# Performance work log

Hardware: AMD Instinct MI355X
Metric: run time of the kernel (lower is better)

The kernel has to match this reference:

```python
import jax, jax.numpy as jnp
import numpy as np


def setup_inputs() -> dict:
    key = jax.random.key(0)
    B, T, H, W = 256, 16, 160, 160
    sms = 2
    N = T * (H // sms) * (W // sms)  # 102400 tokens per sample
    k1, _ = jax.random.split(key)
    soft_scores = jax.random.uniform(k1, (B, N), dtype=jnp.float32)
    image_grid_thw = jnp.tile(jnp.array([T, H, W], dtype=jnp.int64), (B, 1))
    return {
        "soft_scores": soft_scores,
        "image_grid_thw": image_grid_thw,
        "spatial_merge_size": sms,
    }


def reference(soft_scores, image_grid_thw, spatial_merge_size,
              lambda_compact=1.0, lambda_tv=1.0, eps=1e-6):
    if soft_scores.ndim == 3:
        soft_scores = soft_scores[..., 0]
    B = soft_scores.shape[0]
    # Uniform grid across the batch (static shapes) -> vectorize over B.
    thw = np.asarray(image_grid_thw)
    t = int(thw[0, 0])
    h = int(thw[0, 1]) // spatial_merge_size
    w = int(thw[0, 2]) // spatial_merge_size
    n = t * h * w

    # s: [B, t, h, w], clamped at 0 like torch clamp_min(0.0)
    s = jnp.maximum(soft_scores[:, :n].astype(jnp.float32).reshape(B, t, h, w), 0.0)
    tot = jnp.maximum(s.sum(axis=(1, 2, 3), keepdims=True), eps)
    p = s / tot  # per-sample normalized distribution

    yy = jnp.linspace(-1.0, 1.0, h, dtype=jnp.float32).reshape(1, 1, h, 1)
    xx = jnp.linspace(-1.0, 1.0, w, dtype=jnp.float32).reshape(1, 1, 1, w)
    mu_x = (p * xx).sum(axis=(1, 2, 3)).reshape(B, 1, 1, 1)
    mu_y = (p * yy).sum(axis=(1, 2, 3)).reshape(B, 1, 1, 1)
    compact = (p * ((xx - mu_x) ** 2 + (yy - mu_y) ** 2)).sum(axis=(1, 2, 3))  # [B]

    tv = jnp.zeros((B,), dtype=jnp.float32)
    if h > 1:
        tv = tv + jnp.abs(s[:, :, 1:, :] - s[:, :, :-1, :]).mean(axis=(1, 2, 3))
    if w > 1:
        tv = tv + jnp.abs(s[:, :, :, 1:] - s[:, :, :, :-1]).mean(axis=(1, 2, 3))
    if t > 1:
        tv = tv + 0.3 * jnp.abs(s[:, 1:, :, :] - s[:, :-1, :, :]).mean(axis=(1, 2, 3))

    return compact.mean() * lambda_compact + tv.mean() * lambda_tv
```

## Files before the change

kernel.cpp:

```cpp
#include <hip/hip_runtime.h>

#define T_DIM 16
#define H2 80
#define W2 80
#define SLICE (H2 * W2)
#define SAMPLE (T_DIM * SLICE)
#define BANDS 5
#define ROWS_PER_BAND (H2 / BANDS)
#define BLOCK (ROWS_PER_BAND * W2 / 4)

__device__ __forceinline__ float4 relu4(float4 v) {
    v.x = fmaxf(v.x, 0.f); v.y = fmaxf(v.y, 0.f);
    v.z = fmaxf(v.z, 0.f); v.w = fmaxf(v.w, 0.f);
    return v;
}

__global__ __launch_bounds__(BLOCK) void tsr_phase1(const float* __restrict__ scores,
                                                    float* __restrict__ ws) {
    __shared__ float lds[(ROWS_PER_BAND + 1) * W2];
    __shared__ float red[(BLOCK / 64) * 7];

    const int blk  = blockIdx.x;
    const int b    = blk / BANDS;
    const int band = blk % BANDS;
    const int tid  = threadIdx.x;

    const int y0  = band * ROWS_PER_BAND;
    const int r   = tid / (W2 / 4);
    const int cx  = tid % (W2 / 4);
    const int y   = y0 + r;
    const int xb  = cx * 4;
    const int pos = tid * 4;

    const float step = 2.0f / (float)(H2 - 1);
    const float yy  = -1.0f + (float)y * step;
    const float xx0 = -1.0f + (float)(xb + 0) * step;
    const float xx1 = -1.0f + (float)(xb + 1) * step;
    const float xx2 = -1.0f + (float)(xb + 2) * step;
    const float xx3 = -1.0f + (float)(xb + 3) * step;
    const float yy2 = yy * yy;
    const float cq0 = xx0 * xx0 + yy2;
    const float cq1 = xx1 * xx1 + yy2;
    const float cq2 = xx2 * xx2 + yy2;
    const float cq3 = xx3 * xx3 + yy2;

    const float4* base = (const float4*)(scores + (size_t)b * SAMPLE);
    const int f4idx = band * BLOCK + tid;
    const bool halo = (y0 + ROWS_PER_BAND < H2) && (tid < W2 / 4);
    const int haloIdx = (y0 + ROWS_PER_BAND) * (W2 / 4) + tid;

    const bool wavail = (xb + 4 < W2);
    const bool havail = (y + 1 < H2);

    float s0 = 0.f, sx = 0.f, sy = 0.f, sq = 0.f;
    float tvh = 0.f, tvw = 0.f, tvt = 0.f;
    float4 prev = make_float4(0.f, 0.f, 0.f, 0.f);

    float4 v = relu4(base[f4idx]);
    float4 hv = make_float4(0.f, 0.f, 0.f, 0.f);
    if (halo) hv = relu4(base[haloIdx]);

    for (int t = 0; t < T_DIM; ++t) {
        float4 vn = make_float4(0.f, 0.f, 0.f, 0.f);
        float4 hvn = make_float4(0.f, 0.f, 0.f, 0.f);
        if (t + 1 < T_DIM) {
            const float4* sln = base + (size_t)(t + 1) * (SLICE / 4);
            vn = sln[f4idx];
            if (halo) hvn = sln[haloIdx];
        }

        __syncthreads();
        *(float4*)&lds[pos] = v;
        if (halo) *(float4*)&lds[ROWS_PER_BAND * W2 + tid * 4] = hv;
        __syncthreads();

        const float rs = v.x + v.y + v.z + v.w;
        s0 += rs;
        sy = fmaf(yy, rs, sy);
        sx = fmaf(xx0, v.x, sx); sx = fmaf(xx1, v.y, sx);
        sx = fmaf(xx2, v.z, sx); sx = fmaf(xx3, v.w, sx);
        sq = fmaf(cq0, v.x, sq); sq = fmaf(cq1, v.y, sq);
        sq = fmaf(cq2, v.z, sq); sq = fmaf(cq3, v.w, sq);

        tvw += fabsf(v.y - v.x) + fabsf(v.z - v.y) + fabsf(v.w - v.z);
        if (wavail) tvw += fabsf(lds[pos + 4] - v.w);

        if (havail) {
            const float4 d = *(const float4*)&lds[pos + W2];
            tvh += fabsf(d.x - v.x) + fabsf(d.y - v.y) +
                   fabsf(d.z - v.z) + fabsf(d.w - v.w);
        }

        if (t > 0) {
            tvt += fabsf(v.x - prev.x) + fabsf(v.y - prev.y) +
                   fabsf(v.z - prev.z) + fabsf(v.w - prev.w);
        }
        prev = v;

        v = relu4(vn);
        if (halo) hv = relu4(hvn);
    }

    float acc[7] = {s0, sx, sy, sq, tvh, tvw, tvt};
#pragma unroll
    for (int off = 32; off > 0; off >>= 1) {
#pragma unroll
        for (int i = 0; i < 7; ++i) acc[i] += __shfl_down(acc[i], off);
    }
    const int wave = tid >> 6;
    const int lane = tid & 63;
    __syncthreads();
    if (lane == 0) {
#pragma unroll
        for (int i = 0; i < 7; ++i) red[wave * 7 + i] = acc[i];
    }
    __syncthreads();
    if (tid < 7) {
        float s = 0.f;
#pragma unroll
        for (int wv = 0; wv < BLOCK / 64; ++wv) s += red[wv * 7 + tid];
        ws[blk * 8 + tid] = s;
    }
}

__global__ __launch_bounds__(256) void tsr_finalize(const float* __restrict__ ws,
                                                    float* __restrict__ out, int B) {
    __shared__ float red[256];
    const int tid = threadIdx.x;
    float acc = 0.f;
    const float ch = 1.0f / (float)(T_DIM * (H2 - 1) * W2);
    const float cw = 1.0f / (float)(T_DIM * H2 * (W2 - 1));
    const float ct = 0.3f / (float)((T_DIM - 1) * H2 * W2);
    for (int b = tid; b < B; b += 256) {
        float p[7] = {0.f, 0.f, 0.f, 0.f, 0.f, 0.f, 0.f};
        for (int band = 0; band < BANDS; ++band) {
            const float* w = ws + (size_t)(b * BANDS + band) * 8;
#pragma unroll
            for (int i = 0; i < 7; ++i) p[i] += w[i];
        }
        const float S0 = p[0], Sx = p[1], Sy = p[2], Sq = p[3];
        const float Th = p[4], Tw = p[5], Tt = p[6];
        const float tot = fmaxf(S0, 1e-6f);
        const float inv = 1.0f / tot;
        const float mux = Sx * inv, muy = Sy * inv;
        const float m2 = mux * mux + muy * muy;
        const float compact = Sq * inv - 2.0f * m2 + m2 * (S0 * inv);
        const float tv = Th * ch + Tw * cw + Tt * ct;
        acc += compact + tv;
    }
    red[tid] = acc;
    __syncthreads();
    for (int s = 128; s > 0; s >>= 1) {
        if (tid < s) red[tid] += red[tid + s];
        __syncthreads();
    }
    if (tid == 0) out[0] = red[0] / (float)B;
}

extern "C" void kernel_launch(void* const* d_in, const int* in_sizes, int n_in,
                              void* d_out, int out_size, void* d_ws, size_t ws_size,
                              hipStream_t stream) {
    const float* scores = (const float*)d_in[0];
    const int B = in_sizes[0] / SAMPLE;
    float* ws = (float*)d_ws;

    tsr_phase1<<<B * BANDS, BLOCK, 0, stream>>>(scores, ws);
    tsr_finalize<<<1, 256, 0, stream>>>(ws, (float*)d_out, B);
}
```

Measured before the change: 160.0 us.

## Replace LDS neighbor exchange with direct redundant global loads

Drops the shared-memory staging of each time slice and the two barriers per iteration. Each thread now reads its right and down neighbors straight from global memory, relying on cache hits, and uses clamped offsets so the missing edge terms come out as zero without branches. The loop is unrolled by four so loads from several slices can be in flight together. In exchange it issues roughly twice the global load instructions and drops the explicit one-slice-ahead prefetch.

```diff
diff --git a/kernel.cpp b/kernel.cpp
--- a/kernel.cpp
+++ b/kernel.cpp
@@ -17,7 +17,6 @@
 
 __global__ __launch_bounds__(BLOCK) void tsr_phase1(const float* __restrict__ scores,
                                                     float* __restrict__ ws) {
-    __shared__ float lds[(ROWS_PER_BAND + 1) * W2];
     __shared__ float red[(BLOCK / 64) * 7];
 
     const int blk  = blockIdx.x;
@@ -30,7 +29,6 @@
     const int cx  = tid % (W2 / 4);
     const int y   = y0 + r;
     const int xb  = cx * 4;
-    const int pos = tid * 4;
 
     const float step = 2.0f / (float)(H2 - 1);
     const float yy  = -1.0f + (float)y * step;
@@ -44,35 +42,25 @@
     const float cq2 = xx2 * xx2 + yy2;
     const float cq3 = xx3 * xx3 + yy2;
 
-    const float4* base = (const float4*)(scores + (size_t)b * SAMPLE);
-    const int f4idx = band * BLOCK + tid;
-    const bool halo = (y0 + ROWS_PER_BAND < H2) && (tid < W2 / 4);
-    const int haloIdx = (y0 + ROWS_PER_BAND) * (W2 / 4) + tid;
-
-    const bool wavail = (xb + 4 < W2);
-    const bool havail = (y + 1 < H2);
+    const float* sampBase = scores + (size_t)b * SAMPLE;
+    const int rowOff = y * W2 + xb;
+    const int hOff = (y + 1 < H2) ? rowOff + W2 : rowOff;
+    const int wOff = (xb + 4 < W2) ? rowOff + 4 : rowOff + 3;
 
     float s0 = 0.f, sx = 0.f, sy = 0.f, sq = 0.f;
     float tvh = 0.f, tvw = 0.f, tvt = 0.f;
     float4 prev = make_float4(0.f, 0.f, 0.f, 0.f);
 
-    float4 v = relu4(base[f4idx]);
-    float4 hv = make_float4(0.f, 0.f, 0.f, 0.f);
-    if (halo) hv = relu4(base[haloIdx]);
+#pragma unroll 4
+    for (int t = 0; t < T_DIM; ++t) {
+        const float* sl = sampBase + (size_t)t * SLICE;
+        const float4 v4 = *(const float4*)(sl + rowOff);
+        const float4 h4 = *(const float4*)(sl + hOff);
+        const float  wn = sl[wOff];
 
-    for (int t = 0; t < T_DIM; ++t) {
-        float4 vn = make_float4(0.f, 0.f, 0.f, 0.f);
-        float4 hvn = make_float4(0.f, 0.f, 0.f, 0.f);
-        if (t + 1 < T_DIM) {
-            const float4* sln = base + (size_t)(t + 1) * (SLICE / 4);
-            vn = sln[f4idx];
-            if (halo) hvn = sln[haloIdx];
-        }
-
-        __syncthreads();
-        *(float4*)&lds[pos] = v;
-        if (halo) *(float4*)&lds[ROWS_PER_BAND * W2 + tid * 4] = hv;
-        __syncthreads();
+        const float4 v = relu4(v4);
+        const float4 hN = relu4(h4);
+        const float  wN = fmaxf(wn, 0.f);
 
         const float rs = v.x + v.y + v.z + v.w;
         s0 += rs;
@@ -82,23 +70,17 @@
         sq = fmaf(cq0, v.x, sq); sq = fmaf(cq1, v.y, sq);
         sq = fmaf(cq2, v.z, sq); sq = fmaf(cq3, v.w, sq);
 
-        tvw += fabsf(v.y - v.x) + fabsf(v.z - v.y) + fabsf(v.w - v.z);
-        if (wavail) tvw += fabsf(lds[pos + 4] - v.w);
+        tvw += fabsf(v.y - v.x) + fabsf(v.z - v.y) + fabsf(v.w - v.z)
+             + fabsf(wN - v.w);
 
-        if (havail) {
-            const float4 d = *(const float4*)&lds[pos + W2];
-            tvh += fabsf(d.x - v.x) + fabsf(d.y - v.y) +
-                   fabsf(d.z - v.z) + fabsf(d.w - v.w);
-        }
+        tvh += fabsf(hN.x - v.x) + fabsf(hN.y - v.y) +
+               fabsf(hN.z - v.z) + fabsf(hN.w - v.w);
 
         if (t > 0) {
             tvt += fabsf(v.x - prev.x) + fabsf(v.y - prev.y) +
                    fabsf(v.z - prev.z) + fabsf(v.w - prev.w);
         }
         prev = v;
-
-        v = relu4(vn);
-        if (halo) hv = relu4(hvn);
     }
 
     float acc[7] = {s0, sx, sy, sq, tvh, tvw, tvt};
@@ -109,7 +91,6 @@
     }
     const int wave = tid >> 6;
     const int lane = tid & 63;
-    __syncthreads();
     if (lane == 0) {
 #pragma unroll
         for (int i = 0; i < 7; ++i) red[wave * 7 + i] = acc[i];
```

After: 159.2 us. About the same (-0.5%).
